# Performance work log

Measured on AMD Instinct MI355X. Metric: run time of the kernel, lower is better.

Reference implementation:

```python
import jax, jax.numpy as jnp
import numpy as np

B, S, D, H, L = 32, 2048, 256, 256, 2  # batch, seq_len, input_size, hidden_size, num_layers


def setup_inputs() -> dict:
    key = jax.random.key(0)
    ks = jax.random.split(key, 11)
    s = 0.05
    return {
        "x": jax.random.normal(ks[0], (B, S, D), jnp.float32),
        "enc_h": jax.random.normal(ks[1], (B, 2 * H), jnp.float32),
        "enc_c": jax.random.normal(ks[2], (B, 2 * H), jnp.float32),
        # stacked per-layer LSTMCell params, PyTorch gate order (i, f, g, o)
        "Wih_f": jax.random.normal(ks[3], (L, 4 * H, D), jnp.float32) * s,
        "Whh_f": jax.random.normal(ks[4], (L, 4 * H, H), jnp.float32) * s,
        "bih_f": jax.random.normal(ks[5], (L, 4 * H), jnp.float32) * s,
        "bhh_f": jax.random.normal(ks[6], (L, 4 * H), jnp.float32) * s,
        "Wih_b": jax.random.normal(ks[7], (L, 4 * H, D), jnp.float32) * s,
        "Whh_b": jax.random.normal(ks[8], (L, 4 * H, H), jnp.float32) * s,
        "bih_b": jax.random.normal(ks[9], (L, 4 * H), jnp.float32) * s,
        "bhh_b": jax.random.normal(ks[10], (L, 4 * H), jnp.float32) * s,
    }


def _lstm_cell(x, h, c, Wih, Whh, b):
    gates = x @ Wih.T + h @ Whh.T + b  # [B, 4H]
    i, f, g, o = jnp.split(gates, 4, axis=-1)
    c_new = jax.nn.sigmoid(f) * c + jax.nn.sigmoid(i) * jnp.tanh(g)
    h_new = jax.nn.sigmoid(o) * jnp.tanh(c_new)
    return h_new, c_new


def reference(x, enc_h, enc_c, Wih_f, Whh_f, bih_f, bhh_f, Wih_b, Whh_b, bih_b, bhh_b):
    h = enc_h.shape[1] // 2
    nl = Wih_f.shape[0]
    # initial states: same encoder slice replicated to every layer
    hf0 = jnp.broadcast_to(enc_h[:, :h], (nl, enc_h.shape[0], h))
    hb0 = jnp.broadcast_to(enc_h[:, h:], (nl, enc_h.shape[0], h))
    cf0 = jnp.broadcast_to(enc_c[:, :h], (nl, enc_c.shape[0], h))
    cb0 = jnp.broadcast_to(enc_c[:, h:], (nl, enc_c.shape[0], h))

    def step(carry, x_t):
        hf, cf, hb, cb = carry  # each [L, B, H]
        inp_f = x_t
        inp_b = x_t[:, ::-1]  # source flips the FEATURE axis of the timestep
        hfs, cfs, hbs, cbs = [], [], [], []
        for j in range(nl):
            h_f, c_f = _lstm_cell(inp_f, hf[j], cf[j], Wih_f[j], Whh_f[j], bih_f[j] + bhh_f[j])
            h_b, c_b = _lstm_cell(inp_b, hb[j], cb[j], Wih_b[j], Whh_b[j], bih_b[j] + bhh_b[j])
            inp_f, inp_b = h_f, h_b
            hfs.append(h_f); cfs.append(c_f); hbs.append(h_b); cbs.append(c_b)
        new_carry = (jnp.stack(hfs), jnp.stack(cfs), jnp.stack(hbs), jnp.stack(cbs))
        return new_carry, jnp.concatenate([hfs[-1], hbs[-1]], axis=1)  # [B, 2H]

    carry0 = (hf0, cf0, hb0, cb0)
    xs = jnp.swapaxes(x, 0, 1)  # [S, B, D]
    (hf, cf, hb, cb), out = jax.lax.scan(step, carry0, xs)
    out = jnp.swapaxes(out, 0, 1)  # [B, S, 2H]
    h_last = jnp.concatenate([hf[-1], hb[-1]], axis=1)
    c_last = jnp.concatenate([cf[-1], cb[-1]], axis=1)
    return out, (h_last, c_last)
```

## Files before the change

### kernel.cpp

```cpp
#include <hip/hip_runtime.h>


typedef _Float16 half8 __attribute__((ext_vector_type(8)));
typedef float f32x4 __attribute__((ext_vector_type(4)));
typedef unsigned u32x4v __attribute__((ext_vector_type(4)));
typedef unsigned long long ull;

#define B_ 32
#define S_ 2048
#define D_ 256
#define H_ 256
#define G_ 1024
#define OUT0 (B_*S_*2*H_)

#define NSLOT 4
#define PKTROW 128

__device__ __forceinline__ size_t hoff(int chain, int slot, int row, int pkt){
  return ((size_t)((chain*NSLOT + slot)*B_ + row))*PKTROW + pkt;
}

__device__ __forceinline__ float sigmoidf_(float v){ return 1.f/(1.f+__expf(-v)); }
__device__ __forceinline__ float tanhf_(float v){ return 2.f/(1.f+__expf(-2.f*v)) - 1.f; }

__device__ __forceinline__ ull ld_pkt(const ull* p){
  return __hip_atomic_load(p, __ATOMIC_RELAXED, __HIP_MEMORY_SCOPE_SYSTEM);
}
__device__ __forceinline__ void st_pkt(ull* p, ull v){
  __hip_atomic_store(p, v, __ATOMIC_RELAXED, __HIP_MEMORY_SCOPE_SYSTEM);
}

__global__ __launch_bounds__(64) void epoch_bump(unsigned* __restrict__ epoch)
{
  if (threadIdx.x == 0)
    __hip_atomic_fetch_add(epoch, 1u, __ATOMIC_RELAXED, __HIP_MEMORY_SCOPE_SYSTEM);
}

__global__ __launch_bounds__(256) void lstm_prep(const float* __restrict__ enc_h,
                                                 const unsigned* __restrict__ epoch,
                                                 ull* __restrict__ hb)
{
  const unsigned tag0 = __hip_atomic_load(epoch, __ATOMIC_RELAXED,
                                          __HIP_MEMORY_SCOPE_SYSTEM) * 4096u;
  int idx = blockIdx.x*blockDim.x + threadIdx.x;
  for (int j = idx; j < 4*B_*PKTROW; j += gridDim.x*blockDim.x) {
    int pkt   = j & 127;
    int row   = (j >> 7) & 31;
    int chain = j >> 12;
    int dirv  = chain >> 1;
    int col   = pkt*2;
    _Float16 lo = (_Float16)enc_h[row*(2*H_) + dirv*H_ + col];
    _Float16 hi = (_Float16)enc_h[row*(2*H_) + dirv*H_ + col + 1];
    unsigned pair = (unsigned)__builtin_bit_cast(unsigned short, lo)
                  | ((unsigned)__builtin_bit_cast(unsigned short, hi) << 16);
    st_pkt(hb + hoff(chain, 0, row, pkt), ((ull)tag0 << 32) | pair);
  }
}

__global__ __launch_bounds__(64,1) void lstm_main(
    const float* __restrict__ x,
    const float* __restrict__ enc_c,
    const float* __restrict__ Wih_f, const float* __restrict__ Whh_f,
    const float* __restrict__ bih_f, const float* __restrict__ bhh_f,
    const float* __restrict__ Wih_b, const float* __restrict__ Whh_b,
    const float* __restrict__ bih_b, const float* __restrict__ bhh_b,
    float* __restrict__ out,
    const unsigned* __restrict__ epoch,
    ull* __restrict__ hb)
{
  const int bid   = blockIdx.x;
  const int chain = bid & 3;
  const int w     = bid >> 2;
  const int dir   = chain >> 1;
  const int layer = chain & 1;
  const int m     = w & 1;
  const int c0    = (w >> 1) << 4;
  const int lane  = threadIdx.x;
  const int quad  = lane >> 4;
  const int lq    = lane & 15;

  const float* Wih = dir ? Wih_b : Wih_f;
  const float* Whh = dir ? Whh_b : Whh_f;
  const float* bih = dir ? bih_b : bih_f;
  const float* bhh = dir ? bhh_b : bhh_f;

  half8 bf[4][16];
#pragma unroll
  for (int q = 0; q < 4; ++q) {
    const int n_g = q*256 + c0 + lq;
    const float* wihr = Wih + (size_t)layer*G_*256 + (size_t)n_g*256 + quad*8;
    const float* whhr = Whh + (size_t)layer*G_*256 + (size_t)n_g*256 + quad*8;
#pragma unroll
    for (int kk = 0; kk < 16; ++kk) {
      const float* src = (kk < 8) ? (wihr + kk*32) : (whhr + (kk-8)*32);
      f32x4 w0 = *(const f32x4*)src;
      f32x4 w1 = *(const f32x4*)(src+4);
      half8 hv;
      hv[0]=(_Float16)w0[0]; hv[1]=(_Float16)w0[1]; hv[2]=(_Float16)w0[2]; hv[3]=(_Float16)w0[3];
      hv[4]=(_Float16)w1[0]; hv[5]=(_Float16)w1[1]; hv[6]=(_Float16)w1[2]; hv[7]=(_Float16)w1[3];
      bf[q][kk] = hv;
    }
  }

  float bias[4];
#pragma unroll
  for (int q = 0; q < 4; ++q) {
    const int n_g = q*256 + c0 + lq;
    bias[q] = bih[layer*G_ + n_g] + bhh[layer*G_ + n_g];
  }

  f32x4 cst;
#pragma unroll
  for (int r = 0; r < 4; ++r) {
    const int b = m*16 + quad*4 + r;
    cst[r] = enc_c[b*(2*H_) + dir*H_ + c0 + lq];
  }

  const unsigned EB = __hip_atomic_load(epoch, __ATOMIC_RELAXED,
                                        __HIP_MEMORY_SCOPE_SYSTEM) * 4096u;

  const int  pm        = lane & 15;
  const int  probeRow  = m*16 + 15;
  const int  probePkt  = pm*8 + 7;
  const bool probeAlt  = ((lane >> 4) & 1) != 0;

  const int arow = m*16 + lq;
  const float* xrowBase = x + (size_t)arow*S_*D_;

  bool dead = false;

  for (int t = 0; t < S_; ++t) {
    half8 ain[8], arec[8];
    const unsigned tagT = EB + (unsigned)t;

    if (layer == 0) {
      const float* xr = xrowBase + (size_t)t*D_;
#pragma unroll
      for (int kk = 0; kk < 8; ++kk) {
        const int k = kk*32 + quad*8;
        half8 hv;
        if (dir == 0) {
          f32x4 a0 = *(const f32x4*)(xr + k);
          f32x4 a1 = *(const f32x4*)(xr + k + 4);
          hv[0]=(_Float16)a0[0]; hv[1]=(_Float16)a0[1]; hv[2]=(_Float16)a0[2]; hv[3]=(_Float16)a0[3];
          hv[4]=(_Float16)a1[0]; hv[5]=(_Float16)a1[1]; hv[6]=(_Float16)a1[2]; hv[7]=(_Float16)a1[3];
        } else {
          const float* p = xr + (248 - k);
          f32x4 a0 = *(const f32x4*)p;
          f32x4 a1 = *(const f32x4*)(p + 4);
          hv[0]=(_Float16)a1[3]; hv[1]=(_Float16)a1[2]; hv[2]=(_Float16)a1[1]; hv[3]=(_Float16)a1[0];
          hv[4]=(_Float16)a0[3]; hv[5]=(_Float16)a0[2]; hv[6]=(_Float16)a0[1]; hv[7]=(_Float16)a0[0];
        }
        ain[kk] = hv;
      }
    }

    {
      const ull* pp;
      unsigned want;
      bool isGE = false;
      if (layer == 0) {
        if (!probeAlt) { pp = hb + hoff(chain,   t&3,     probeRow, probePkt); want = tagT; }
        else           { pp = hb + hoff(chain+1, (t+1)&3, probeRow, probePkt); want = tagT - 3; isGE = true; }
      } else {
        if (!probeAlt) { pp = hb + hoff(chain,   t&3,     probeRow, probePkt); want = tagT; }
        else           { pp = hb + hoff(chain-1, (t+1)&3, probeRow, probePkt); want = tagT + 1; }
      }
      int guard = 0;
      while (true) {
        unsigned tg = (unsigned)(ld_pkt(pp) >> 32);
        bool ok = isGE ? ((t < 3) || ((int)(tg - want) >= 0)) : (tg == want);
        if (__all(ok)) break;
        if (++guard > (1 << 19)) { dead = true; break; }
      }
      if (dead) break;
    }

    {
      int guard = 0;
      while (true) {
        bool ok = true;
#pragma unroll
        for (int kk = 0; kk < 8; ++kk) {
          const ull* p4 = hb + hoff(chain, t&3, arow, kk*16 + quad*4);
          ull p0 = ld_pkt(p4+0), p1 = ld_pkt(p4+1), p2 = ld_pkt(p4+2), p3 = ld_pkt(p4+3);
          ok &= ((unsigned)(p0>>32) == tagT) & ((unsigned)(p1>>32) == tagT)
              & ((unsigned)(p2>>32) == tagT) & ((unsigned)(p3>>32) == tagT);
          u32x4v d = { (unsigned)p0, (unsigned)p1, (unsigned)p2, (unsigned)p3 };
          arec[kk] = __builtin_bit_cast(half8, d);
        }
        if (layer == 1) {
          const unsigned tagU = tagT + 1;
#pragma unroll
          for (int kk = 0; kk < 8; ++kk) {
            const ull* p4 = hb + hoff(chain-1, (t+1)&3, arow, kk*16 + quad*4);
            ull p0 = ld_pkt(p4+0), p1 = ld_pkt(p4+1), p2 = ld_pkt(p4+2), p3 = ld_pkt(p4+3);
            ok &= ((unsigned)(p0>>32) == tagU) & ((unsigned)(p1>>32) == tagU)
                & ((unsigned)(p2>>32) == tagU) & ((unsigned)(p3>>32) == tagU);
            u32x4v d = { (unsigned)p0, (unsigned)p1, (unsigned)p2, (unsigned)p3 };
            ain[kk] = __builtin_bit_cast(half8, d);
          }
        }
        if (__all(ok)) break;
        if (++guard > (1 << 16)) { dead = true; break; }
      }
      if (dead) break;
    }

    f32x4 acc0 = {bias[0],bias[0],bias[0],bias[0]};
    f32x4 acc1 = {bias[1],bias[1],bias[1],bias[1]};
    f32x4 acc2 = {bias[2],bias[2],bias[2],bias[2]};
    f32x4 acc3 = {bias[3],bias[3],bias[3],bias[3]};
#pragma unroll
    for (int kk = 0; kk < 8; ++kk) {
      acc0 = __builtin_amdgcn_mfma_f32_16x16x32_f16(ain[kk], bf[0][kk], acc0, 0,0,0);
      acc1 = __builtin_amdgcn_mfma_f32_16x16x32_f16(ain[kk], bf[1][kk], acc1, 0,0,0);
      acc2 = __builtin_amdgcn_mfma_f32_16x16x32_f16(ain[kk], bf[2][kk], acc2, 0,0,0);
      acc3 = __builtin_amdgcn_mfma_f32_16x16x32_f16(ain[kk], bf[3][kk], acc3, 0,0,0);
    }
#pragma unroll
    for (int kk = 0; kk < 8; ++kk) {
      acc0 = __builtin_amdgcn_mfma_f32_16x16x32_f16(arec[kk], bf[0][kk+8], acc0, 0,0,0);
      acc1 = __builtin_amdgcn_mfma_f32_16x16x32_f16(arec[kk], bf[1][kk+8], acc1, 0,0,0);
      acc2 = __builtin_amdgcn_mfma_f32_16x16x32_f16(arec[kk], bf[2][kk+8], acc2, 0,0,0);
      acc3 = __builtin_amdgcn_mfma_f32_16x16x32_f16(arec[kk], bf[3][kk+8], acc3, 0,0,0);
    }

    float hval[4];
#pragma unroll
    for (int r = 0; r < 4; ++r) {
      float si = sigmoidf_(acc0[r]);
      float sf = sigmoidf_(acc1[r]);
      float tg = tanhf_  (acc2[r]);
      float so = sigmoidf_(acc3[r]);
      float cn = sf*cst[r] + si*tg;
      cst[r] = cn;
      hval[r] = so*tanhf_(cn);
    }

    {
      const unsigned tagN = tagT + 1;
#pragma unroll
      for (int r = 0; r < 4; ++r) {
        float partner = __shfl_xor(hval[r], 1);
        if (!(lq & 1)) {
          unsigned short lo = __builtin_bit_cast(unsigned short, (_Float16)hval[r]);
          unsigned short hi = __builtin_bit_cast(unsigned short, (_Float16)partner);
          unsigned pair = (unsigned)lo | ((unsigned)hi << 16);
          const int row = m*16 + quad*4 + r;
          const int pkt = (c0 + lq) >> 1;
          st_pkt(hb + hoff(chain, (t+1)&3, row, pkt), ((ull)tagN << 32) | pair);
        }
      }
    }

    if (layer == 1) {
      const int colg = dir*256 + c0 + lq;
#pragma unroll
      for (int r = 0; r < 4; ++r) {
        const int b = m*16 + quad*4 + r;
        out[((size_t)b*S_ + t)*(2*H_) + colg] = hval[r];
      }
      if (t == S_-1) {
#pragma unroll
        for (int r = 0; r < 4; ++r) {
          const int b = m*16 + quad*4 + r;
          out[OUT0 + (size_t)b*(2*H_) + colg] = hval[r];
          out[OUT0 + B_*2*H_ + (size_t)b*(2*H_) + colg] = cst[r];
        }
      }
    }
  }
}

extern "C" void kernel_launch(void* const* d_in, const int* in_sizes, int n_in,
                              void* d_out, int out_size, void* d_ws, size_t ws_size,
                              hipStream_t stream) {
  const float* x     = (const float*)d_in[0];
  const float* enc_h = (const float*)d_in[1];
  const float* enc_c = (const float*)d_in[2];
  const float* Wih_f = (const float*)d_in[3];
  const float* Whh_f = (const float*)d_in[4];
  const float* bih_f = (const float*)d_in[5];
  const float* bhh_f = (const float*)d_in[6];
  const float* Wih_b = (const float*)d_in[7];
  const float* Whh_b = (const float*)d_in[8];
  const float* bih_b = (const float*)d_in[9];
  const float* bhh_b = (const float*)d_in[10];

  unsigned* epoch = (unsigned*)((char*)d_ws + 16384);
  ull* hb         = (ull*)((char*)d_ws + 32768);

  epoch_bump<<<1, 64, 0, stream>>>(epoch);
  lstm_prep<<<64, 256, 0, stream>>>(enc_h, epoch, hb);
  lstm_main<<<128, 64, 0, stream>>>(x, enc_c, Wih_f, Whh_f, bih_f, bhh_f,
                                    Wih_b, Whh_b, bih_b, bhh_b,
                                    (float*)d_out, epoch, hb);
}
```

Measured before the change: 14.10 ms.

## Pin each LSTM chain to one XCD and exchange hidden state via L2-scoped flags

Result: slower. 24.42 ms (+73.2%).

```diff
diff --git a/kernel.cpp b/kernel.cpp
--- a/kernel.cpp
+++ b/kernel.cpp
@@ -3,7 +3,7 @@
 
 typedef _Float16 half8 __attribute__((ext_vector_type(8)));
 typedef float f32x4 __attribute__((ext_vector_type(4)));
-typedef unsigned u32x4v __attribute__((ext_vector_type(4)));
+typedef unsigned u32x4 __attribute__((ext_vector_type(4)));
 typedef unsigned long long ull;
 
 #define B_ 32
@@ -13,76 +13,130 @@
 #define G_ 1024
 #define OUT0 (B_*S_*2*H_)
 
-#define NSLOT 4
-#define PKTROW 128
-
-__device__ __forceinline__ size_t hoff(int chain, int slot, int row, int pkt){
-  return ((size_t)((chain*NSLOT + slot)*B_ + row))*PKTROW + pkt;
+#define HL2_SLOTS 2
+#define HSY_SLOTS 4
+
+__device__ __forceinline__ size_t l2off(int chain,int s,int row,int pkt){
+  return ((size_t)(((chain*HL2_SLOTS)+s)*B_ + row)*128 + pkt)*8;
+}
+__device__ __forceinline__ size_t syoff(int dir,int s,int row,int pkt){
+  return ((size_t)(((dir*HSY_SLOTS)+s)*B_ + row)*128 + pkt)*8;
 }
 
 __device__ __forceinline__ float sigmoidf_(float v){ return 1.f/(1.f+__expf(-v)); }
 __device__ __forceinline__ float tanhf_(float v){ return 2.f/(1.f+__expf(-2.f*v)) - 1.f; }
 
-__device__ __forceinline__ ull ld_pkt(const ull* p){
-  return __hip_atomic_load(p, __ATOMIC_RELAXED, __HIP_MEMORY_SCOPE_SYSTEM);
-}
-__device__ __forceinline__ void st_pkt(ull* p, ull v){
-  __hip_atomic_store(p, v, __ATOMIC_RELAXED, __HIP_MEMORY_SCOPE_SYSTEM);
-}
-
-__global__ __launch_bounds__(64) void epoch_bump(unsigned* __restrict__ epoch)
+template<bool FAST>
+__device__ __forceinline__ ull ld_probe(const void* p){
+  ull v;
+  if constexpr (FAST)
+    asm volatile("global_load_dwordx2 %0, %1, off sc0\n\ts_waitcnt vmcnt(0)"
+                 : "=v"(v) : "v"(p) : "memory");
+  else
+    asm volatile("global_load_dwordx2 %0, %1, off sc0 sc1\n\ts_waitcnt vmcnt(0)"
+                 : "=v"(v) : "v"(p) : "memory");
+  return v;
+}
+
+#define LD16(SCOPE) \
+  asm volatile( \
+    "global_load_dwordx4 %0, %16, off " SCOPE "\n\t" \
+    "global_load_dwordx4 %1, %16, off offset:16 " SCOPE "\n\t" \
+    "global_load_dwordx4 %2, %16, off offset:128 " SCOPE "\n\t" \
+    "global_load_dwordx4 %3, %16, off offset:144 " SCOPE "\n\t" \
+    "global_load_dwordx4 %4, %16, off offset:256 " SCOPE "\n\t" \
+    "global_load_dwordx4 %5, %16, off offset:272 " SCOPE "\n\t" \
+    "global_load_dwordx4 %6, %16, off offset:384 " SCOPE "\n\t" \
+    "global_load_dwordx4 %7, %16, off offset:400 " SCOPE "\n\t" \
+    "global_load_dwordx4 %8, %16, off offset:512 " SCOPE "\n\t" \
+    "global_load_dwordx4 %9, %16, off offset:528 " SCOPE "\n\t" \
+    "global_load_dwordx4 %10, %16, off offset:640 " SCOPE "\n\t" \
+    "global_load_dwordx4 %11, %16, off offset:656 " SCOPE "\n\t" \
+    "global_load_dwordx4 %12, %16, off offset:768 " SCOPE "\n\t" \
+    "global_load_dwordx4 %13, %16, off offset:784 " SCOPE "\n\t" \
+    "global_load_dwordx4 %14, %16, off offset:896 " SCOPE "\n\t" \
+    "global_load_dwordx4 %15, %16, off offset:912 " SCOPE \
+    : "=&v"(g[0]),"=&v"(g[1]),"=&v"(g[2]),"=&v"(g[3]), \
+      "=&v"(g[4]),"=&v"(g[5]),"=&v"(g[6]),"=&v"(g[7]), \
+      "=&v"(g[8]),"=&v"(g[9]),"=&v"(g[10]),"=&v"(g[11]), \
+      "=&v"(g[12]),"=&v"(g[13]),"=&v"(g[14]),"=&v"(g[15]) \
+    : "v"(p) : "memory")
+
+template<bool FAST>
+__device__ __forceinline__ void ld_bulk16(const void* p, u32x4 g[16]){
+  if constexpr (FAST) { LD16("sc0"); } else { LD16("sc0 sc1"); }
+}
+
+template<bool FAST>
+__device__ __forceinline__ void st_pub4(void* p, ull p0, ull p1, ull p2, ull p3){
+  if constexpr (FAST)
+    asm volatile(
+      "global_store_dwordx2 %0, %1, off sc0\n\t"
+      "global_store_dwordx2 %0, %2, off offset:1024 sc0\n\t"
+      "global_store_dwordx2 %0, %3, off offset:2048 sc0\n\t"
+      "global_store_dwordx2 %0, %4, off offset:3072 sc0"
+      :: "v"(p),"v"(p0),"v"(p1),"v"(p2),"v"(p3) : "memory");
+  else
+    asm volatile(
+      "global_store_dwordx2 %0, %1, off sc0 sc1\n\t"
+      "global_store_dwordx2 %0, %2, off offset:1024 sc0 sc1\n\t"
+      "global_store_dwordx2 %0, %3, off offset:2048 sc0 sc1\n\t"
+      "global_store_dwordx2 %0, %4, off offset:3072 sc0 sc1"
+      :: "v"(p),"v"(p0),"v"(p1),"v"(p2),"v"(p3) : "memory");
+}
+
+__device__ __forceinline__ void st_tok(void* p, unsigned v){
+  asm volatile("global_store_dword %0, %1, off sc0" :: "v"(p), "v"(v) : "memory");
+}
+__device__ __forceinline__ int ld_tok(const void* p){
+  int v;
+  asm volatile("global_load_dword %0, %1, off sc0\n\ts_waitcnt vmcnt(0)"
+               : "=v"(v) : "v"(p) : "memory");
+  return v;
+}
+
+__device__ __forceinline__ bool verify16(const u32x4 g[16], unsigned tag){
+  bool ok = true;
+#pragma unroll
+  for (int i = 0; i < 16; ++i) ok &= (g[i][1] == tag) & (g[i][3] == tag);
+  return ok;
+}
+
+__global__ __launch_bounds__(64) void lstm_prep(int* __restrict__ cnt,
+                                                int* __restrict__ agg,
+                                                int* __restrict__ verd,
+                                                unsigned* __restrict__ epoch)
 {
-  if (threadIdx.x == 0)
+  int i = threadIdx.x;
+  if (i == 0)
     __hip_atomic_fetch_add(epoch, 1u, __ATOMIC_RELAXED, __HIP_MEMORY_SCOPE_SYSTEM);
-}
-
-__global__ __launch_bounds__(256) void lstm_prep(const float* __restrict__ enc_h,
-                                                 const unsigned* __restrict__ epoch,
-                                                 ull* __restrict__ hb)
+  if (i < 4) {
+    __hip_atomic_store(&cnt[i*16], 0, __ATOMIC_RELAXED, __HIP_MEMORY_SCOPE_SYSTEM);
+    __hip_atomic_store(&agg[i*16], 0, __ATOMIC_RELAXED, __HIP_MEMORY_SCOPE_SYSTEM);
+  }
+  if (i < 32)
+    __hip_atomic_store(&verd[i*16], -1, __ATOMIC_RELAXED, __HIP_MEMORY_SCOPE_SYSTEM);
+}
+
+template<bool FAST>
+__device__ __forceinline__ void run_chain(
+    const float* __restrict__ x, const float* __restrict__ enc_h,
+    const float* __restrict__ enc_c,
+    const float* __restrict__ Wih, const float* __restrict__ Whh,
+    const float* __restrict__ bih, const float* __restrict__ bhh,
+    float* __restrict__ out, int* __restrict__ agg,
+    char* __restrict__ hbL2, char* __restrict__ hbSys,
+    unsigned EB, int chain, int mb, int tid)
 {
-  const unsigned tag0 = __hip_atomic_load(epoch, __ATOMIC_RELAXED,
-                                          __HIP_MEMORY_SCOPE_SYSTEM) * 4096u;
-  int idx = blockIdx.x*blockDim.x + threadIdx.x;
-  for (int j = idx; j < 4*B_*PKTROW; j += gridDim.x*blockDim.x) {
-    int pkt   = j & 127;
-    int row   = (j >> 7) & 31;
-    int chain = j >> 12;
-    int dirv  = chain >> 1;
-    int col   = pkt*2;
-    _Float16 lo = (_Float16)enc_h[row*(2*H_) + dirv*H_ + col];
-    _Float16 hi = (_Float16)enc_h[row*(2*H_) + dirv*H_ + col + 1];
-    unsigned pair = (unsigned)__builtin_bit_cast(unsigned short, lo)
-                  | ((unsigned)__builtin_bit_cast(unsigned short, hi) << 16);
-    st_pkt(hb + hoff(chain, 0, row, pkt), ((ull)tag0 << 32) | pair);
-  }
-}
-
-__global__ __launch_bounds__(64,1) void lstm_main(
-    const float* __restrict__ x,
-    const float* __restrict__ enc_c,
-    const float* __restrict__ Wih_f, const float* __restrict__ Whh_f,
-    const float* __restrict__ bih_f, const float* __restrict__ bhh_f,
-    const float* __restrict__ Wih_b, const float* __restrict__ Whh_b,
-    const float* __restrict__ bih_b, const float* __restrict__ bhh_b,
-    float* __restrict__ out,
-    const unsigned* __restrict__ epoch,
-    ull* __restrict__ hb)
-{
-  const int bid   = blockIdx.x;
-  const int chain = bid & 3;
-  const int w     = bid >> 2;
   const int dir   = chain >> 1;
   const int layer = chain & 1;
-  const int m     = w & 1;
-  const int c0    = (w >> 1) << 4;
-  const int lane  = threadIdx.x;
+  const int m     = mb & 1;
+  const int wv    = tid >> 6;
+  const int cg    = (mb >> 1)*4 + wv;
+  const int c0    = cg << 4;
+  const int lane  = tid & 63;
   const int quad  = lane >> 4;
   const int lq    = lane & 15;
-
-  const float* Wih = dir ? Wih_b : Wih_f;
-  const float* Whh = dir ? Whh_b : Whh_f;
-  const float* bih = dir ? bih_b : bih_f;
-  const float* bhh = dir ? bhh_b : bhh_f;
 
   half8 bf[4][16];
 #pragma unroll
@@ -116,22 +170,37 @@
     cst[r] = enc_c[b*(2*H_) + dir*H_ + c0 + lq];
   }
 
-  const unsigned EB = __hip_atomic_load(epoch, __ATOMIC_RELAXED,
-                                        __HIP_MEMORY_SCOPE_SYSTEM) * 4096u;
-
-  const int  pm        = lane & 15;
-  const int  probeRow  = m*16 + 15;
-  const int  probePkt  = pm*8 + 7;
-  const bool probeAlt  = ((lane >> 4) & 1) != 0;
-
   const int arow = m*16 + lq;
   const float* xrowBase = x + (size_t)arow*S_*D_;
+  int* aggP = agg + (dir*2 + m)*16;
+
+  {
+    const int pkt = cg*8 + (lq >> 1);
+    if (!(lq & 1)) {
+      ull pk[4];
+#pragma unroll
+      for (int r = 0; r < 4; ++r) {
+        const int b = m*16 + quad*4 + r;
+        const int col = c0 + lq;
+        _Float16 lo = (_Float16)enc_h[b*(2*H_) + dir*H_ + col];
+        _Float16 hi = (_Float16)enc_h[b*(2*H_) + dir*H_ + col + 1];
+        unsigned pair = (unsigned)__builtin_bit_cast(unsigned short, lo)
+                      | ((unsigned)__builtin_bit_cast(unsigned short, hi) << 16);
+        pk[r] = ((ull)EB << 32) | pair;
+      }
+      st_pub4<FAST>(hbL2 + l2off(chain, 0, m*16 + quad*4, pkt), pk[0],pk[1],pk[2],pk[3]);
+    }
+  }
+
+  u32x4 gA[16], gB[16];
+  if (layer == 1)
+    ld_bulk16<false>(hbSys + syoff(dir, 1, arow, quad*4), gB);
 
   bool dead = false;
 
   for (int t = 0; t < S_; ++t) {
+    const unsigned tagT = EB + (unsigned)t;
     half8 ain[8], arec[8];
-    const unsigned tagT = EB + (unsigned)t;
 
     if (layer == 0) {
       const float* xr = xrowBase + (size_t)t*D_;
@@ -156,55 +225,58 @@
     }
 
     {
-      const ull* pp;
-      unsigned want;
-      bool isGE = false;
-      if (layer == 0) {
-        if (!probeAlt) { pp = hb + hoff(chain,   t&3,     probeRow, probePkt); want = tagT; }
-        else           { pp = hb + hoff(chain+1, (t+1)&3, probeRow, probePkt); want = tagT - 3; isGE = true; }
-      } else {
-        if (!probeAlt) { pp = hb + hoff(chain,   t&3,     probeRow, probePkt); want = tagT; }
-        else           { pp = hb + hoff(chain-1, (t+1)&3, probeRow, probePkt); want = tagT + 1; }
-      }
+      const void* pp = hbL2 + l2off(chain, t & 1, m*16 + 15, (lane & 15)*8 + 7);
       int guard = 0;
-      while (true) {
-        unsigned tg = (unsigned)(ld_pkt(pp) >> 32);
-        bool ok = isGE ? ((t < 3) || ((int)(tg - want) >= 0)) : (tg == want);
-        if (__all(ok)) break;
-        if (++guard > (1 << 19)) { dead = true; break; }
+      for (;;) {
+        ull v = ld_probe<FAST>(pp);
+        if (__all((unsigned)(v >> 32) == tagT)) break;
+        if (++guard > (1 << 20)) { dead = true; break; }
+      }
+    }
+    if (dead) break;
+    __builtin_amdgcn_sched_barrier(0);
+
+    if (layer == 1) {
+      if (cg == 0 && lane == 0)
+        __hip_atomic_store(aggP, t, __ATOMIC_RELAXED, __HIP_MEMORY_SCOPE_SYSTEM);
+    } else {
+      if (!(t & 1)) {
+        int guard = 0;
+        while (__hip_atomic_load(aggP, __ATOMIC_RELAXED, __HIP_MEMORY_SCOPE_SYSTEM) < t - 2) {
+          if (++guard > (1 << 20)) { dead = true; break; }
+        }
+        if (dead) break;
+      }
+    }
+
+    bool okB = (layer == 0) || verify16(gB, tagT + 1);
+    {
+      const void* lb = hbL2 + l2off(chain, t & 1, arow, quad*4);
+      const void* ub = hbSys + syoff(dir, (t + 1) & 3, arow, quad*4);
+      int guard = 0;
+      for (;;) {
+        ld_bulk16<FAST>(lb, gA);
+        if (!okB) ld_bulk16<false>(ub, gB);
+        asm volatile("s_waitcnt vmcnt(0)" ::: "memory");
+        __builtin_amdgcn_sched_barrier(0);
+        bool ok = verify16(gA, tagT);
+        if (!okB) okB = verify16(gB, tagT + 1);
+        if (__all(ok & okB)) break;
+        if (++guard > (1 << 20)) { dead = true; break; }
       }
       if (dead) break;
     }
-
-    {
-      int guard = 0;
-      while (true) {
-        bool ok = true;
-#pragma unroll
-        for (int kk = 0; kk < 8; ++kk) {
-          const ull* p4 = hb + hoff(chain, t&3, arow, kk*16 + quad*4);
-          ull p0 = ld_pkt(p4+0), p1 = ld_pkt(p4+1), p2 = ld_pkt(p4+2), p3 = ld_pkt(p4+3);
-          ok &= ((unsigned)(p0>>32) == tagT) & ((unsigned)(p1>>32) == tagT)
-              & ((unsigned)(p2>>32) == tagT) & ((unsigned)(p3>>32) == tagT);
-          u32x4v d = { (unsigned)p0, (unsigned)p1, (unsigned)p2, (unsigned)p3 };
-          arec[kk] = __builtin_bit_cast(half8, d);
-        }
-        if (layer == 1) {
-          const unsigned tagU = tagT + 1;
-#pragma unroll
-          for (int kk = 0; kk < 8; ++kk) {
-            const ull* p4 = hb + hoff(chain-1, (t+1)&3, arow, kk*16 + quad*4);
-            ull p0 = ld_pkt(p4+0), p1 = ld_pkt(p4+1), p2 = ld_pkt(p4+2), p3 = ld_pkt(p4+3);
-            ok &= ((unsigned)(p0>>32) == tagU) & ((unsigned)(p1>>32) == tagU)
-                & ((unsigned)(p2>>32) == tagU) & ((unsigned)(p3>>32) == tagU);
-            u32x4v d = { (unsigned)p0, (unsigned)p1, (unsigned)p2, (unsigned)p3 };
-            ain[kk] = __builtin_bit_cast(half8, d);
-          }
-        }
-        if (__all(ok)) break;
-        if (++guard > (1 << 16)) { dead = true; break; }
-      }
-      if (dead) break;
+#pragma unroll
+    for (int kk = 0; kk < 8; ++kk) {
+      u32x4 d = { gA[2*kk][0], gA[2*kk][2], gA[2*kk+1][0], gA[2*kk+1][2] };
+      arec[kk] = __builtin_bit_cast(half8, d);
+    }
+    if (layer == 1) {
+#pragma unroll
+      for (int kk = 0; kk < 8; ++kk) {
+        u32x4 d = { gB[2*kk][0], gB[2*kk][2], gB[2*kk+1][0], gB[2*kk+1][2] };
+        ain[kk] = __builtin_bit_cast(half8, d);
+      }
     }
 
     f32x4 acc0 = {bias[0],bias[0],bias[0],bias[0]};
@@ -240,21 +312,27 @@
 
     {
       const unsigned tagN = tagT + 1;
+      ull pk[4];
 #pragma unroll
       for (int r = 0; r < 4; ++r) {
         float partner = __shfl_xor(hval[r], 1);
-        if (!(lq & 1)) {
-          unsigned short lo = __builtin_bit_cast(unsigned short, (_Float16)hval[r]);
-          unsigned short hi = __builtin_bit_cast(unsigned short, (_Float16)partner);
-          unsigned pair = (unsigned)lo | ((unsigned)hi << 16);
-          const int row = m*16 + quad*4 + r;
-          const int pkt = (c0 + lq) >> 1;
-          st_pkt(hb + hoff(chain, (t+1)&3, row, pkt), ((ull)tagN << 32) | pair);
-        }
+        unsigned short lo = __builtin_bit_cast(unsigned short, (_Float16)hval[r]);
+        unsigned short hi = __builtin_bit_cast(unsigned short, (_Float16)partner);
+        pk[r] = ((ull)tagN << 32) | ((unsigned)lo | ((unsigned)hi << 16));
+      }
+      if (!(lq & 1)) {
+        const int pkt = cg*8 + (lq >> 1);
+        st_pub4<FAST>(hbL2 + l2off(chain, (t+1) & 1, m*16 + quad*4, pkt),
+                      pk[0],pk[1],pk[2],pk[3]);
+        if (layer == 0)
+          st_pub4<false>(hbSys + syoff(dir, (t+1) & 3, m*16 + quad*4, pkt),
+                         pk[0],pk[1],pk[2],pk[3]);
       }
     }
 
     if (layer == 1) {
+      if (t < S_-1)
+        ld_bulk16<false>(hbSys + syoff(dir, (t + 2) & 3, arow, quad*4), gB);
       const int colg = dir*256 + c0 + lq;
 #pragma unroll
       for (int r = 0; r < 4; ++r) {
@@ -271,6 +349,88 @@
       }
     }
   }
+}
+
+__global__ __launch_bounds__(256,1) void lstm_main(
+    const float* __restrict__ x,
+    const float* __restrict__ enc_h,
+    const float* __restrict__ enc_c,
+    const float* __restrict__ Wih_f, const float* __restrict__ Whh_f,
+    const float* __restrict__ bih_f, const float* __restrict__ bhh_f,
+    const float* __restrict__ Wih_b, const float* __restrict__ Whh_b,
+    const float* __restrict__ bih_b, const float* __restrict__ bhh_b,
+    float* __restrict__ out,
+    int* __restrict__ cnt, int* __restrict__ agg,
+    int* __restrict__ verd, int* __restrict__ toks,
+    unsigned* __restrict__ epoch,
+    char* __restrict__ hbL2, char* __restrict__ hbSys)
+{
+  __shared__ int sXcc, sTk, sFast;
+  const int tid = threadIdx.x;
+
+  if (tid == 0) {
+    unsigned xcc;
+    asm volatile("s_getreg_b32 %0, hwreg(HW_REG_XCC_ID)" : "=s"(xcc));
+    xcc &= 7;
+    int tk = 999;
+    if (xcc < 4)
+      tk = __hip_atomic_fetch_add(&cnt[xcc*16], 1, __ATOMIC_RELAXED,
+                                  __HIP_MEMORY_SCOPE_SYSTEM);
+    sXcc = (int)xcc; sTk = tk;
+  }
+  __syncthreads();
+  const int chain = sXcc;
+  const int mb    = sTk;
+  if (chain >= 4 || mb >= 8) return;
+
+  const unsigned E = __hip_atomic_load(epoch, __ATOMIC_RELAXED,
+                                       __HIP_MEMORY_SCOPE_SYSTEM);
+
+  if (tid < 64) {
+    bool ok = true;
+#pragma unroll 1
+    for (int phase = 1; phase <= 2; ++phase) {
+      const unsigned tgt = E*2u + (unsigned)phase;
+      if (tid == 0) st_tok(&toks[(chain*8 + mb)*16], tgt);
+      int guard = 0;
+      for (;;) {
+        int v = ld_tok(&toks[(chain*8 + (tid & 7))*16]);
+        if (__all((int)((unsigned)v - tgt) >= 0)) break;
+        if (++guard > (1 << 15)) { ok = false; break; }
+      }
+      if (!ok) break;
+    }
+    if (tid == 0)
+      __hip_atomic_store(&verd[(chain*8 + mb)*16], ok ? 1 : 0,
+                         __ATOMIC_RELAXED, __HIP_MEMORY_SCOPE_SYSTEM);
+    int vd = -1; bool have = true;
+    {
+      int guard = 0;
+      for (;;) {
+        vd = __hip_atomic_load(&verd[(chain*8 + (tid & 7))*16],
+                               __ATOMIC_RELAXED, __HIP_MEMORY_SCOPE_SYSTEM);
+        if (__all(vd >= 0)) break;
+        if (++guard > (1 << 20)) { have = false; break; }
+      }
+    }
+    if (tid == 0) sFast = (have && __all(vd == 1)) ? 1 : 0;
+  }
+  __syncthreads();
+  const bool fast = (sFast != 0);
+
+  const int dir = chain >> 1;
+  const float* Wih = dir ? Wih_b : Wih_f;
+  const float* Whh = dir ? Whh_b : Whh_f;
+  const float* bih = dir ? bih_b : bih_f;
+  const float* bhh = dir ? bhh_b : bhh_f;
+  const unsigned EB = E * 4096u;
+
+  if (fast)
+    run_chain<true >(x, enc_h, enc_c, Wih, Whh, bih, bhh, out, agg,
+                     hbL2, hbSys, EB, chain, mb, tid);
+  else
+    run_chain<false>(x, enc_h, enc_c, Wih, Whh, bih, bhh, out, agg,
+                     hbL2, hbSys, EB, chain, mb, tid);
 }
 
 extern "C" void kernel_launch(void* const* d_in, const int* in_sizes, int n_in,
@@ -288,12 +448,18 @@
   const float* bih_b = (const float*)d_in[9];
   const float* bhh_b = (const float*)d_in[10];
 
-  unsigned* epoch = (unsigned*)((char*)d_ws + 16384);
-  ull* hb         = (ull*)((char*)d_ws + 32768);
-
-  epoch_bump<<<1, 64, 0, stream>>>(epoch);
-  lstm_prep<<<64, 256, 0, stream>>>(enc_h, epoch, hb);
-  lstm_main<<<128, 64, 0, stream>>>(x, enc_c, Wih_f, Whh_f, bih_f, bhh_f,
-                                    Wih_b, Whh_b, bih_b, bhh_b,
-                                    (float*)d_out, epoch, hb);
-}
+  int*      cnt   = (int*)d_ws;
+  int*      agg   = (int*)((char*)d_ws + 1024);
+  int*      verd  = (int*)((char*)d_ws + 2048);
+  int*      toks  = (int*)((char*)d_ws + 4096);
+  unsigned* epoch = (unsigned*)((char*)d_ws + 8192);
+  char*     hbL2  = (char*)d_ws + 32768;
+  char*     hbSys = (char*)d_ws + 32768 + 262144;
+
+  lstm_prep<<<1, 64, 0, stream>>>(cnt, agg, verd, epoch);
+  lstm_main<<<512, 256, 0, stream>>>(x, enc_h, enc_c,
+                                     Wih_f, Whh_f, bih_f, bhh_f,
+                                     Wih_b, Whh_b, bih_b, bhh_b,
+                                     (float*)d_out,
+                                     cnt, agg, verd, toks, epoch, hbL2, hbSys);
+}
```
